# Optimization experiments

Measured on AMD Instinct MI355X. Metric: run time of the kernel, lower is better.

## Reference

```python
import jax, jax.numpy as jnp
import numpy as np

IMG = 128          # img_size
P = 8              # patch_size
H = 768            # model dim (hidden_size)
E = 1536           # GAU expansion dim (2*H), u/v width
K = 128            # key_size
L = (IMG // P) ** 2   # 256 patches
PD = P * P * 3        # 192 patch dim
T = 1000
NL = 24


def sinusoidal_embeddings(pos, dim, base):
    # pos: (L,) -> (L, dim) = [sin | cos]
    half = dim // 2
    freqs = jnp.exp(jnp.arange(half, dtype=jnp.float32) * (-np.log(base) / (half - 1)))
    ang = pos[:, None].astype(jnp.float32) * freqs[None, :]
    return jnp.concatenate([jnp.sin(ang), jnp.cos(ang)], axis=-1)


def make_rope_2d():
    w = IMG // P
    pos = jnp.arange(w * w)
    emb1 = sinusoidal_embeddings(pos // w, 64, 1000.0)
    emb2 = sinusoidal_embeddings(pos % w, 64, 1000.0)
    return jnp.concatenate([emb1, emb2], axis=-1)[None]  # (1, L, 128)


def apply_rope(x, pe):
    # faithful to source: sin_emb = pe[..., :d/2], cos_emb = pe[..., d/2:]
    d = pe.shape[-1]
    sin = pe[..., : d // 2]
    cos = pe[..., d // 2 :]
    x1 = x[..., : d // 2]
    x2 = x[..., d // 2 : d]
    return jnp.concatenate([x1 * cos - x2 * sin, x2 * cos + x1 * sin], axis=-1)


def rmsnorm(x, w):
    rms = jnp.sqrt(jnp.mean(x * x, axis=-1, keepdims=True))
    return x / (rms + 1e-6) * w


def setup_inputs() -> dict:
    key = jax.random.key(0)
    ks = jax.random.split(key, 9)
    B = 16
    s = 0.02
    return {
        "x": jax.random.normal(ks[0], (B, 3, IMG, IMG), dtype=jnp.float32),
        "t_idx": jax.random.randint(ks[1], (B, 1), 0, T),
        "patch_W": jax.random.normal(ks[2], (PD, H), dtype=jnp.float32) * s,
        "t_emb": jax.random.normal(ks[3], (T, H), dtype=jnp.float32) * s,
        "Wuv": jax.random.normal(ks[4], (NL, H, 2 * E + 2 * K), dtype=jnp.float32) * s,
        "Wout": jax.random.normal(ks[5], (NL, E, H), dtype=jnp.float32) * s,
        "gnorm": jnp.ones((NL, H), dtype=jnp.float32),
        "fnorm_w": jnp.ones((H,), dtype=jnp.float32),
        "unpatch_W": jax.random.normal(ks[6], (H, PD), dtype=jnp.float32) * s,
    }


def reference(x, t_idx, patch_W, t_emb, Wuv, Wout, gnorm, fnorm_w, unpatch_W):
    B = x.shape[0]
    g = IMG // P
    # patchify: (B,3,128,128) -> (B, 256, 192)
    xp = x.reshape(B, 3, g, P, g, P).transpose(0, 2, 4, 3, 5, 1).reshape(B, L, PD)
    h = xp @ patch_W + t_emb[t_idx[:, 0]][:, None, :]   # (B, L, H)
    pe = make_rope_2d()                                  # (1, L, 128)
    scale = K ** (-0.5)

    def block(h, params):
        wuv, wout, gn = params
        xn = rmsnorm(h, gn)
        uvqk = xn @ wuv                                  # (B, L, 2E+2K)
        u = jax.nn.silu(uvqk[..., :E])
        v = jax.nn.silu(uvqk[..., E : 2 * E])
        q = apply_rope(uvqk[..., 2 * E : 2 * E + K], pe)
        k = apply_rope(uvqk[..., 2 * E + K :], pe)
        attn = jax.nn.softmax(jnp.einsum('blk,bmk->blm', q, k) * scale, axis=-1)
        o = u * jnp.einsum('blm,bme->ble', attn, v)      # (B, L, E)
        return h + o @ wout, None

    h, _ = jax.lax.scan(block, h, (Wuv, Wout, gnorm))
    h = rmsnorm(h, fnorm_w) @ unpatch_W                  # (B, L, PD)
    # unpatchify: (B,256,192) -> (B,3,128,128)
    out = h.reshape(B, g, g, P, P, 3).transpose(0, 5, 1, 3, 2, 4).reshape(B, 3, IMG, IMG)
    return out
```

## Files before the change

kernel.cpp:

```cpp
#include <hip/hip_runtime.h>
#include <math.h>

#define IMG   128
#define Hdim  768
#define Edim  1536
#define Ltok  256
#define PDim  192
#define NLAY  24
#define Bsz   16
#define Mrows 4096
#define UVW   3328

typedef __bf16 bf16x8 __attribute__((ext_vector_type(8)));
typedef float  f32x4  __attribute__((ext_vector_type(4)));

__device__ __forceinline__ unsigned short f2b(float f) {
    unsigned int u = __float_as_uint(f);
    unsigned int r = (u + 0x7FFF + ((u >> 16) & 1)) >> 16;
    return (unsigned short)r;
}
__device__ __forceinline__ float b2f(unsigned short s) {
    return __uint_as_float((unsigned int)s << 16);
}
__device__ __forceinline__ unsigned int pk2(float lo, float hi) {
    return (unsigned int)f2b(lo) | ((unsigned int)f2b(hi) << 16);
}
__device__ __forceinline__ float silu(float x) {
    return x / (1.0f + expf(-x));
}
__device__ __forceinline__ void gload16(const void* g, void* l) {
    __builtin_amdgcn_global_load_lds(
        (const __attribute__((address_space(1))) void*)g,
        (__attribute__((address_space(3))) void*)l, 16, 0, 0);
}
__device__ __forceinline__ int xcd_wg() {
    int nwg = gridDim.x;
    int orig = blockIdx.x;
    int q8 = nwg >> 3, r8 = nwg & 7;
    int xcd = orig & 7, loc = orig >> 3;
    return (xcd < r8 ? xcd * (q8 + 1) : r8 * (q8 + 1) + (xcd - r8) * q8) + loc;
}

__global__ void pe_kernel(float* __restrict__ pe) {
    int l = blockIdx.x;
    int j = threadIdx.x;
    const float c = -logf(1000.0f) / 31.0f;
    int   sub = j & 31;
    float f   = expf(c * (float)sub);
    float pos = (j < 64) ? (float)(l >> 4) : (float)(l & 15);
    float ang = pos * f;
    pe[l * 128 + j] = ((j & 32) == 0) ? sinf(ang) : cosf(ang);
}

__global__ void patchify_kernel(const float* __restrict__ x, unsigned short* __restrict__ xp) {
    int bc = blockIdx.x;
    int iy = bc & 127;
    int t  = bc >> 7;
    int c  = t % 3;
    int b  = t / 3;
    int ix = threadIdx.x;
    float v = x[((size_t)(b * 3 + c) * IMG + iy) * IMG + ix];
    int gy = iy >> 3, py = iy & 7, gx = ix >> 3, px = ix & 7;
    xp[(size_t)(b * Ltok + gy * 16 + gx) * PDim + (py * 8 + px) * 3 + c] = f2b(v);
}

__global__ void trans_kernel(const float* __restrict__ src, int ldS, long long sS,
                             unsigned short* __restrict__ dst, int ldD, long long sD) {
    src += (long long)blockIdx.z * sS;
    dst += (long long)blockIdx.z * sD;
    __shared__ float t[32][33];
    int c0 = blockIdx.x * 32, r0 = blockIdx.y * 32;
    int tx = threadIdx.x, ty = threadIdx.y;
#pragma unroll
    for (int i = 0; i < 4; ++i)
        t[ty + 8 * i][tx] = src[(size_t)(r0 + ty + 8 * i) * ldS + c0 + tx];
    __syncthreads();
#pragma unroll
    for (int i = 0; i < 4; ++i)
        dst[(size_t)(c0 + ty + 8 * i) * ldD + r0 + tx] = f2b(t[tx][ty + 8 * i]);
}

template <int ACC>
__launch_bounds__(256)
__global__ void gemm_bf16(const unsigned short* __restrict__ A, int lda,
                          const unsigned short* __restrict__ Bt, int ldb,
                          float* __restrict__ C, int ldc,
                          int Kt, int Nt, int nbx) {
    __shared__ unsigned short lsA[2][4096];
    __shared__ unsigned short lsB[2][4096];
    int wg = xcd_wg();
    int bx = wg % nbx, by = wg / nbx;
    int tid  = threadIdx.x;
    int lane = tid & 63, w = tid >> 6, wr = w >> 1, wc = w & 1;
    int row0 = by * 128, col0 = bx * 128;
    int fr = lane & 15, fk = (lane >> 4) * 8;
    f32x4 acc[4][4] = {};

    int c0 = tid, c1 = tid + 256;
    int ar0 = row0 + (c0 >> 2), ar1 = row0 + (c1 >> 2);
    int bn0 = col0 + (c0 >> 2), bn1 = col0 + (c1 >> 2);
    if (bn0 > Nt - 1) bn0 = Nt - 1;
    if (bn1 > Nt - 1) bn1 = Nt - 1;
    int ka0 = (c0 & 3) * 8, ka1 = (c1 & 3) * 8;

#define STAGE_G(buf, k0)                                                       \
    gload16(A  + (size_t)ar0 * lda + (k0) + ka0, &lsA[buf][c0 * 8]);           \
    gload16(A  + (size_t)ar1 * lda + (k0) + ka1, &lsA[buf][c1 * 8]);           \
    gload16(Bt + (size_t)bn0 * ldb + (k0) + ka0, &lsB[buf][c0 * 8]);           \
    gload16(Bt + (size_t)bn1 * ldb + (k0) + ka1, &lsB[buf][c1 * 8]);

    STAGE_G(0, 0);
    __syncthreads();
    int nt = Kt >> 5, cur = 0;
    for (int t = 0; t < nt; ++t) {
        if (t + 1 < nt) { STAGE_G(cur ^ 1, (t + 1) * 32); }
        bf16x8 af[4], bfr[4];
#pragma unroll
        for (int m = 0; m < 4; ++m)
            af[m] = *(const bf16x8*)(&lsA[cur][(wr * 64 + m * 16 + fr) * 32 + fk]);
#pragma unroll
        for (int n = 0; n < 4; ++n)
            bfr[n] = *(const bf16x8*)(&lsB[cur][(wc * 64 + n * 16 + fr) * 32 + fk]);
#pragma unroll
        for (int m = 0; m < 4; ++m)
#pragma unroll
            for (int n = 0; n < 4; ++n)
                acc[m][n] = __builtin_amdgcn_mfma_f32_16x16x32_bf16(af[m], bfr[n], acc[m][n], 0, 0, 0);
        __syncthreads();
        cur ^= 1;
    }
#undef STAGE_G

    int crow = (lane >> 4) * 4;
#pragma unroll
    for (int m = 0; m < 4; ++m) {
#pragma unroll
        for (int n = 0; n < 4; ++n) {
            int gc = col0 + wc * 64 + n * 16 + fr;
            if (gc >= Nt) continue;
#pragma unroll
            for (int j = 0; j < 4; ++j) {
                size_t idx = (size_t)(row0 + wr * 64 + m * 16 + crow + j) * ldc + gc;
                if (ACC) C[idx] += acc[m][n][j];
                else     C[idx]  = acc[m][n][j];
            }
        }
    }
}

__launch_bounds__(256)
__global__ void gemm_wout(const unsigned short* __restrict__ A,
                          const unsigned short* __restrict__ Bt,
                          unsigned short* __restrict__ P) {
    __shared__ unsigned short lsA[2][4096];
    __shared__ unsigned short lsB[2][4096];
    int wg = xcd_wg();
    int sk = wg / 192, rem = wg % 192;
    int bx = rem % 6, by = rem / 6;
    int koff = sk * 384;
    unsigned short* C = P + (size_t)sk * Mrows * Hdim;
    int tid  = threadIdx.x;
    int lane = tid & 63, w = tid >> 6, wr = w >> 1, wc = w & 1;
    int row0 = by * 128, col0 = bx * 128;
    int fr = lane & 15, fk = (lane >> 4) * 8;
    f32x4 acc[4][4] = {};

    int c0 = tid, c1 = tid + 256;
    int ar0 = row0 + (c0 >> 2), ar1 = row0 + (c1 >> 2);
    int bn0 = col0 + (c0 >> 2), bn1 = col0 + (c1 >> 2);
    int ka0 = koff + (c0 & 3) * 8, ka1 = koff + (c1 & 3) * 8;

#define STAGE_W(buf, k0)                                                       \
    gload16(A  + (size_t)ar0 * Edim + (k0) + ka0, &lsA[buf][c0 * 8]);          \
    gload16(A  + (size_t)ar1 * Edim + (k0) + ka1, &lsA[buf][c1 * 8]);          \
    gload16(Bt + (size_t)bn0 * Edim + (k0) + ka0, &lsB[buf][c0 * 8]);          \
    gload16(Bt + (size_t)bn1 * Edim + (k0) + ka1, &lsB[buf][c1 * 8]);

    STAGE_W(0, 0);
    __syncthreads();
    int cur = 0;
    for (int t = 0; t < 12; ++t) {
        if (t + 1 < 12) { STAGE_W(cur ^ 1, (t + 1) * 32); }
        bf16x8 af[4], bfr[4];
#pragma unroll
        for (int m = 0; m < 4; ++m)
            af[m] = *(const bf16x8*)(&lsA[cur][(wr * 64 + m * 16 + fr) * 32 + fk]);
#pragma unroll
        for (int n = 0; n < 4; ++n)
            bfr[n] = *(const bf16x8*)(&lsB[cur][(wc * 64 + n * 16 + fr) * 32 + fk]);
#pragma unroll
        for (int m = 0; m < 4; ++m)
#pragma unroll
            for (int n = 0; n < 4; ++n)
                acc[m][n] = __builtin_amdgcn_mfma_f32_16x16x32_bf16(af[m], bfr[n], acc[m][n], 0, 0, 0);
        __syncthreads();
        cur ^= 1;
    }
#undef STAGE_W

    int crow = (lane >> 4) * 4;
#pragma unroll
    for (int m = 0; m < 4; ++m) {
#pragma unroll
        for (int n = 0; n < 4; ++n) {
            int gc = col0 + wc * 64 + n * 16 + fr;
#pragma unroll
            for (int j = 0; j < 4; ++j)
                C[(size_t)(row0 + wr * 64 + m * 16 + crow + j) * Hdim + gc] = f2b(acc[m][n][j]);
        }
    }
}

__global__ __launch_bounds__(512, 2)
void gemm_uvqk8(const unsigned short* __restrict__ A,
                const unsigned short* __restrict__ Bt,
                unsigned short* __restrict__ uT,
                unsigned short* __restrict__ vT,
                unsigned short* __restrict__ qh,
                unsigned short* __restrict__ kh,
                const float* __restrict__ pe) {
    __shared__ char smem[131072];
    int wg = xcd_wg();
    int bx = wg % 13, by = wg / 13;
    int tid = threadIdx.x, lane = tid & 63, wid = tid >> 6;
    int wm = wid >> 2, wn = wid & 3;
    int row0 = by * 256, col0 = bx * 256;
    int fr = lane & 15, hi = lane >> 4;
    f32x4 acc[8][4] = {};

    int d0 = tid * 16, d1 = d0 + 8192;
    int s0 = d0 ^ (((d0 >> 7) & 7) << 4);
    int s1 = d1 ^ (((d1 >> 7) & 7) << 4);
    int sr0 = s0 >> 7, sc0 = (s0 & 127) >> 1;
    int sr1 = s1 >> 7, sc1 = (s1 & 127) >> 1;

#define STG_A(bufo, h, kt) do {                                                            \
    gload16(A + (size_t)(row0 + (h) * 128 + sr0) * Hdim + (kt) * 64 + sc0,                 \
            smem + (bufo) + (h) * 16384 + d0);                                             \
    gload16(A + (size_t)(row0 + (h) * 128 + sr1) * Hdim + (kt) * 64 + sc1,                 \
            smem + (bufo) + (h) * 16384 + d1); } while (0)
#define STG_B(bufo, h, kt) do {                                                            \
    gload16(Bt + (size_t)(col0 + (h) * 128 + sr0) * Hdim + (kt) * 64 + sc0,                \
            smem + (bufo) + 32768 + (h) * 16384 + d0);                                     \
    gload16(Bt + (size_t)(col0 + (h) * 128 + sr1) * Hdim + (kt) * 64 + sc1,                \
            smem + (bufo) + 32768 + (h) * 16384 + d1); } while (0)

    int axor = (fr & 7) << 4;
    int abase = wm * 16384 + fr * 128;
    int bbase = 32768 + (wn >> 1) * 16384 + ((wn & 1) * 64 + fr) * 128;
    int koff0 = (hi * 16) ^ axor;
    int koff1 = (hi * 16 + 64) ^ axor;

    STG_A(0, 0, 0); STG_A(0, 1, 0); STG_B(0, 0, 0); STG_B(0, 1, 0);
    STG_A(65536, 0, 1); STG_A(65536, 1, 1);
    asm volatile("s_waitcnt vmcnt(4)" ::: "memory");
    __builtin_amdgcn_s_barrier();
    __builtin_amdgcn_sched_barrier(0);

    bf16x8 af[4][2], bf0[2][2], bf1[2][2];
    const int NKT = Hdim / 64;
    for (int kt = 0; kt < NKT; ++kt) {
        int curo = (kt & 1) << 16, nxto = curo ^ 65536;
        const char* bufc = smem + curo;

#pragma unroll
        for (int m = 0; m < 4; ++m) {
            af[m][0] = *(const bf16x8*)(bufc + abase + m * 2048 + koff0);
            af[m][1] = *(const bf16x8*)(bufc + abase + m * 2048 + koff1);
        }
#pragma unroll
        for (int n = 0; n < 2; ++n) {
            bf0[n][0] = *(const bf16x8*)(bufc + bbase + n * 2048 + koff0);
            bf0[n][1] = *(const bf16x8*)(bufc + bbase + n * 2048 + koff1);
        }
        if (kt + 1 < NKT) STG_B(nxto, 0, kt + 1);
        __builtin_amdgcn_s_setprio(1);
#pragma unroll
        for (int m = 0; m < 4; ++m)
#pragma unroll
            for (int n = 0; n < 2; ++n) {
                acc[m][n] = __builtin_amdgcn_mfma_f32_16x16x32_bf16(af[m][0], bf0[n][0], acc[m][n], 0, 0, 0);
                acc[m][n] = __builtin_amdgcn_mfma_f32_16x16x32_bf16(af[m][1], bf0[n][1], acc[m][n], 0, 0, 0);
            }
        __builtin_amdgcn_s_setprio(0);
        __builtin_amdgcn_s_barrier();
        __builtin_amdgcn_sched_barrier(0);

#pragma unroll
        for (int n = 0; n < 2; ++n) {
            bf1[n][0] = *(const bf16x8*)(bufc + bbase + (n + 2) * 2048 + koff0);
            bf1[n][1] = *(const bf16x8*)(bufc + bbase + (n + 2) * 2048 + koff1);
        }
        if (kt + 1 < NKT) STG_B(nxto, 1, kt + 1);
        __builtin_amdgcn_s_setprio(1);
#pragma unroll
        for (int m = 0; m < 4; ++m)
#pragma unroll
            for (int n = 0; n < 2; ++n) {
                acc[m][n + 2] = __builtin_amdgcn_mfma_f32_16x16x32_bf16(af[m][0], bf1[n][0], acc[m][n + 2], 0, 0, 0);
                acc[m][n + 2] = __builtin_amdgcn_mfma_f32_16x16x32_bf16(af[m][1], bf1[n][1], acc[m][n + 2], 0, 0, 0);
            }
        __builtin_amdgcn_s_setprio(0);
        __builtin_amdgcn_s_barrier();
        __builtin_amdgcn_sched_barrier(0);

#pragma unroll
        for (int m = 0; m < 4; ++m) {
            af[m][0] = *(const bf16x8*)(bufc + abase + (m + 4) * 2048 + koff0);
            af[m][1] = *(const bf16x8*)(bufc + abase + (m + 4) * 2048 + koff1);
        }
        __builtin_amdgcn_s_setprio(1);
#pragma unroll
        for (int m = 0; m < 4; ++m)
#pragma unroll
            for (int n = 0; n < 2; ++n) {
                acc[m + 4][n] = __builtin_amdgcn_mfma_f32_16x16x32_bf16(af[m][0], bf0[n][0], acc[m + 4][n], 0, 0, 0);
                acc[m + 4][n] = __builtin_amdgcn_mfma_f32_16x16x32_bf16(af[m][1], bf0[n][1], acc[m + 4][n], 0, 0, 0);
            }
        __builtin_amdgcn_s_setprio(0);
        __builtin_amdgcn_s_barrier();
        __builtin_amdgcn_sched_barrier(0);

        if (kt + 2 < NKT) { STG_A(curo, 0, kt + 2); STG_A(curo, 1, kt + 2); }
        __builtin_amdgcn_s_setprio(1);
#pragma unroll
        for (int m = 0; m < 4; ++m)
#pragma unroll
            for (int n = 0; n < 2; ++n) {
                acc[m + 4][n + 2] = __builtin_amdgcn_mfma_f32_16x16x32_bf16(af[m][0], bf1[n][0], acc[m + 4][n + 2], 0, 0, 0);
                acc[m + 4][n + 2] = __builtin_amdgcn_mfma_f32_16x16x32_bf16(af[m][1], bf1[n][1], acc[m + 4][n + 2], 0, 0, 0);
            }
        __builtin_amdgcn_s_setprio(0);
        asm volatile("s_waitcnt vmcnt(4)" ::: "memory");
        __builtin_amdgcn_s_barrier();
        __builtin_amdgcn_sched_barrier(0);
    }
#undef STG_A
#undef STG_B

    if (bx == 12) {
        float* S = (float*)smem;
        const float qscale = 0.08838834764831845f;
#pragma unroll
        for (int p = 0; p < 4; ++p) {
            __syncthreads();
            if (wm == (p >> 1)) {
#pragma unroll
                for (int m = 0; m < 4; ++m) {
                    int mf = (p & 1) * 4 + m;
                    int rl = m * 16 + hi * 4;
#pragma unroll
                    for (int n = 0; n < 4; ++n) {
                        int cl = wn * 64 + n * 16 + fr;
#pragma unroll
                        for (int j = 0; j < 4; ++j)
                            S[(rl + j) * 256 + cl] = acc[mf][n][j];
                    }
                }
            }
            __syncthreads();
            int r = tid >> 3;
            int dbase = (tid & 7) * 8;
            int row_g = row0 + p * 64 + r;
            int l = row_g & 255;
#pragma unroll
            for (int i = 0; i < 8; ++i) {
                int d = dbase + i;
                float sn = pe[l * 128 + d], cs = pe[l * 128 + 64 + d];
                float q1 = S[r * 256 + d],       q2 = S[r * 256 + d + 64];
                float k1 = S[r * 256 + d + 128], k2 = S[r * 256 + d + 192];
                qh[(size_t)row_g * 128 + d]      = f2b((q1 * cs - q2 * sn) * qscale);
                qh[(size_t)row_g * 128 + d + 64] = f2b((q2 * cs + q1 * sn) * qscale);
                kh[(size_t)row_g * 128 + d]      = f2b(k1 * cs - k2 * sn);
                kh[(size_t)row_g * 128 + d + 64] = f2b(k2 * cs + k1 * sn);
            }
        }
        return;
    }

    __syncthreads();
#pragma unroll
    for (int mf = 0; mf < 8; ++mf) {
        int m_l = wm * 128 + mf * 16 + hi * 4;
#pragma unroll
        for (int nf = 0; nf < 4; ++nf) {
            int e_l = wn * 64 + nf * 16 + fr;
            ushort4 pk;
            pk.x = f2b(silu(acc[mf][nf][0]));
            pk.y = f2b(silu(acc[mf][nf][1]));
            pk.z = f2b(silu(acc[mf][nf][2]));
            pk.w = f2b(silu(acc[mf][nf][3]));
            int byte = (e_l * 512 + m_l * 2) ^ ((e_l & 7) << 4);
            *(ushort4*)(smem + byte) = pk;
        }
    }
    __syncthreads();
    int er = tid >> 5;
    int ch = (tid & 31) * 16;
#pragma unroll
    for (int it = 0; it < 16; ++it) {
        int e_l = it * 16 + er;
        int byte = (e_l * 512 + ch) ^ ((e_l & 7) << 4);
        int4 v = *(const int4*)(smem + byte);
        unsigned short* dst;
        if (bx < 6) {
            dst = uT + (size_t)(col0 + e_l) * Mrows + row0;
        } else {
            int e = col0 + e_l - Edim;
            dst = vT + ((size_t)(row0 >> 8) * Edim + e) * Ltok;
        }
        *(int4*)((char*)dst + ch) = v;
    }
}

__launch_bounds__(256)
__global__ void fused_attn(const unsigned short* __restrict__ qh,
                           const unsigned short* __restrict__ kh,
                           const unsigned short* __restrict__ vT,
                           const unsigned short* __restrict__ uT,
                           unsigned short* __restrict__ ob) {
    int ec = blockIdx.x, qt = blockIdx.y, b = blockIdx.z;
    int tid  = threadIdx.x;
    int lane = tid & 63, w = tid >> 6;
    int fr = lane & 15, hi = lane >> 4;
    int qbase = b * 256 + qt * 64 + w * 16;

    bf16x8 qf[4];
#pragma unroll
    for (int ks = 0; ks < 4; ++ks)
        qf[ks] = *(const bf16x8*)(qh + (size_t)(qbase + fr) * 128 + ks * 32 + hi * 8);
    f32x4 sacc[16] = {};
#pragma unroll
    for (int mf = 0; mf < 16; ++mf) {
#pragma unroll
        for (int ks = 0; ks < 4; ++ks) {
            bf16x8 kf = *(const bf16x8*)(kh + (size_t)(b * 256 + mf * 16 + fr) * 128 + ks * 32 + hi * 8);
            sacc[mf] = __builtin_amdgcn_mfma_f32_16x16x32_bf16(kf, qf[ks], sacc[mf], 0, 0, 0);
        }
    }

    float mx = -3.4e38f;
#pragma unroll
    for (int mf = 0; mf < 16; ++mf)
#pragma unroll
        for (int j = 0; j < 4; ++j)
            mx = fmaxf(mx, sacc[mf][j]);
    mx = fmaxf(mx, __shfl_xor(mx, 16, 64));
    mx = fmaxf(mx, __shfl_xor(mx, 32, 64));
    float sum = 0.f;
#pragma unroll
    for (int mf = 0; mf < 16; ++mf)
#pragma unroll
        for (int j = 0; j < 4; ++j) {
            float e = expf(sacc[mf][j] - mx);
            sacc[mf][j] = e;
            sum += e;
        }
    sum += __shfl_xor(sum, 16, 64);
    sum += __shfl_xor(sum, 32, 64);
    float inv = 1.0f / sum;

    unsigned int dw[16][2];
#pragma unroll
    for (int mf = 0; mf < 16; ++mf) {
        dw[mf][0] = pk2(sacc[mf][0] * inv, sacc[mf][1] * inv);
        dw[mf][1] = pk2(sacc[mf][2] * inv, sacc[mf][3] * inv);
    }

    int sA = fr + 32 * (hi & 1);
    int sB = sA + 16;
    bool up = (hi >> 1) != 0;
    unsigned int pa[8][4];
#pragma unroll
    for (int ks = 0; ks < 8; ++ks) {
        unsigned int a00 = __shfl((int)dw[2 * ks][0],     sA, 64);
        unsigned int a01 = __shfl((int)dw[2 * ks + 1][0], sA, 64);
        unsigned int a10 = __shfl((int)dw[2 * ks][1],     sA, 64);
        unsigned int a11 = __shfl((int)dw[2 * ks + 1][1], sA, 64);
        unsigned int b00 = __shfl((int)dw[2 * ks][0],     sB, 64);
        unsigned int b01 = __shfl((int)dw[2 * ks + 1][0], sB, 64);
        unsigned int b10 = __shfl((int)dw[2 * ks][1],     sB, 64);
        unsigned int b11 = __shfl((int)dw[2 * ks + 1][1], sB, 64);
        pa[ks][0] = up ? a01 : a00;
        pa[ks][1] = up ? a11 : a10;
        pa[ks][2] = up ? b01 : b00;
        pa[ks][3] = up ? b11 : b10;
    }

    const unsigned short* vb = vT + (size_t)b * Edim * Ltok;
    int e0 = ec * 192;
#pragma unroll 2
    for (int ef = 0; ef < 12; ++ef) {
        int e = e0 + ef * 16 + fr;
        f32x4 oacc = {};
#pragma unroll
        for (int ks = 0; ks < 8; ++ks) {
            bf16x8 vf = *(const bf16x8*)(vb + (size_t)e * Ltok + ks * 32 + hi * 8);
            oacc = __builtin_amdgcn_mfma_f32_16x16x32_bf16(*(const bf16x8*)&pa[ks], vf, oacc, 0, 0, 0);
        }
        ushort4 uv = *(const ushort4*)(uT + (size_t)e * Mrows + qbase + hi * 4);
        ob[(size_t)(qbase + hi * 4 + 0) * Edim + e] = f2b(oacc[0] * b2f(uv.x));
        ob[(size_t)(qbase + hi * 4 + 1) * Edim + e] = f2b(oacc[1] * b2f(uv.y));
        ob[(size_t)(qbase + hi * 4 + 2) * Edim + e] = f2b(oacc[2] * b2f(uv.z));
        ob[(size_t)(qbase + hi * 4 + 3) * Edim + e] = f2b(oacc[3] * b2f(uv.w));
    }
}

__global__ void rmsnorm_bias(float* __restrict__ x, const float* __restrict__ t_emb,
                             const int* __restrict__ t_idx, const float* __restrict__ w,
                             unsigned short* __restrict__ y) {
    int r = blockIdx.x * 4 + (threadIdx.x >> 6);
    int lane = threadIdx.x & 63;
    const float* e = t_emb + (size_t)t_idx[r >> 8] * Hdim;
    float* xr = x + (size_t)r * Hdim;
    float4 a = *(const float4*)&xr[lane * 4];
    float4 b = *(const float4*)&xr[lane * 4 + 256];
    float4 c = *(const float4*)&xr[lane * 4 + 512];
    float4 ea = *(const float4*)&e[lane * 4];
    float4 eb = *(const float4*)&e[lane * 4 + 256];
    float4 ec = *(const float4*)&e[lane * 4 + 512];
    a.x += ea.x; a.y += ea.y; a.z += ea.z; a.w += ea.w;
    b.x += eb.x; b.y += eb.y; b.z += eb.z; b.w += eb.w;
    c.x += ec.x; c.y += ec.y; c.z += ec.z; c.w += ec.w;
    *(float4*)&xr[lane * 4]       = a;
    *(float4*)&xr[lane * 4 + 256] = b;
    *(float4*)&xr[lane * 4 + 512] = c;
    float ss = a.x * a.x + a.y * a.y + a.z * a.z + a.w * a.w
             + b.x * b.x + b.y * b.y + b.z * b.z + b.w * b.w
             + c.x * c.x + c.y * c.y + c.z * c.z + c.w * c.w;
#pragma unroll
    for (int o = 1; o < 64; o <<= 1) ss += __shfl_xor(ss, o, 64);
    float s = 1.0f / (sqrtf(ss / (float)Hdim) + 1e-6f);
    float4 wa = *(const float4*)&w[lane * 4];
    float4 wb = *(const float4*)&w[lane * 4 + 256];
    float4 wc = *(const float4*)&w[lane * 4 + 512];
    unsigned short* yr = y + (size_t)r * Hdim;
    ushort4 o0, o1, o2;
    o0.x = f2b(a.x * s * wa.x); o0.y = f2b(a.y * s * wa.y);
    o0.z = f2b(a.z * s * wa.z); o0.w = f2b(a.w * s * wa.w);
    o1.x = f2b(b.x * s * wb.x); o1.y = f2b(b.y * s * wb.y);
    o1.z = f2b(b.z * s * wb.z); o1.w = f2b(b.w * s * wb.w);
    o2.x = f2b(c.x * s * wc.x); o2.y = f2b(c.y * s * wc.y);
    o2.z = f2b(c.z * s * wc.z); o2.w = f2b(c.w * s * wc.w);
    *(ushort4*)&yr[lane * 4]       = o0;
    *(ushort4*)&yr[lane * 4 + 256] = o1;
    *(ushort4*)&yr[lane * 4 + 512] = o2;
}

__global__ void rmsnorm_acc(float* __restrict__ x, const unsigned short* __restrict__ p,
                            const float* __restrict__ w, unsigned short* __restrict__ y) {
    int r = blockIdx.x * 4 + (threadIdx.x >> 6);
    int lane = threadIdx.x & 63;
    float* xr = x + (size_t)r * Hdim;
    float4 a = *(const float4*)&xr[lane * 4];
    float4 b = *(const float4*)&xr[lane * 4 + 256];
    float4 c = *(const float4*)&xr[lane * 4 + 512];
#pragma unroll
    for (int s = 0; s < 4; ++s) {
        const unsigned short* ps = p + (size_t)(s * Mrows + r) * Hdim;
        ushort4 a0 = *(const ushort4*)&ps[lane * 4];
        ushort4 b0 = *(const ushort4*)&ps[lane * 4 + 256];
        ushort4 c0 = *(const ushort4*)&ps[lane * 4 + 512];
        a.x += b2f(a0.x); a.y += b2f(a0.y); a.z += b2f(a0.z); a.w += b2f(a0.w);
        b.x += b2f(b0.x); b.y += b2f(b0.y); b.z += b2f(b0.z); b.w += b2f(b0.w);
        c.x += b2f(c0.x); c.y += b2f(c0.y); c.z += b2f(c0.z); c.w += b2f(c0.w);
    }
    *(float4*)&xr[lane * 4]       = a;
    *(float4*)&xr[lane * 4 + 256] = b;
    *(float4*)&xr[lane * 4 + 512] = c;
    float ss = a.x * a.x + a.y * a.y + a.z * a.z + a.w * a.w
             + b.x * b.x + b.y * b.y + b.z * b.z + b.w * b.w
             + c.x * c.x + c.y * c.y + c.z * c.z + c.w * c.w;
#pragma unroll
    for (int o = 1; o < 64; o <<= 1) ss += __shfl_xor(ss, o, 64);
    float s = 1.0f / (sqrtf(ss / (float)Hdim) + 1e-6f);
    float4 wa = *(const float4*)&w[lane * 4];
    float4 wb = *(const float4*)&w[lane * 4 + 256];
    float4 wc = *(const float4*)&w[lane * 4 + 512];
    unsigned short* yr = y + (size_t)r * Hdim;
    ushort4 o0, o1, o2;
    o0.x = f2b(a.x * s * wa.x); o0.y = f2b(a.y * s * wa.y);
    o0.z = f2b(a.z * s * wa.z); o0.w = f2b(a.w * s * wa.w);
    o1.x = f2b(b.x * s * wb.x); o1.y = f2b(b.y * s * wb.y);
    o1.z = f2b(b.z * s * wb.z); o1.w = f2b(b.w * s * wb.w);
    o2.x = f2b(c.x * s * wc.x); o2.y = f2b(c.y * s * wc.y);
    o2.z = f2b(c.z * s * wc.z); o2.w = f2b(c.w * s * wc.w);
    *(ushort4*)&yr[lane * 4]       = o0;
    *(ushort4*)&yr[lane * 4 + 256] = o1;
    *(ushort4*)&yr[lane * 4 + 512] = o2;
}

__global__ void unpatch_kernel(const float* __restrict__ y, float* __restrict__ out) {
    int bc = blockIdx.x;
    int iy = bc & 127;
    int t  = bc >> 7;
    int c  = t % 3;
    int b  = t / 3;
    int ix = threadIdx.x;
    int gy = iy >> 3, py = iy & 7, gx = ix >> 3, px = ix & 7;
    out[((size_t)(b * 3 + c) * IMG + iy) * IMG + ix] =
        y[(size_t)(b * Ltok + gy * 16 + gx) * PDim + (py * 8 + px) * 3 + c];
}

extern "C" void kernel_launch(void* const* d_in, const int* in_sizes, int n_in,
                              void* d_out, int out_size, void* d_ws, size_t ws_size,
                              hipStream_t stream) {
    const float* x        = (const float*)d_in[0];
    const int*   t_idx    = (const int*)  d_in[1];
    const float* patch_W  = (const float*)d_in[2];
    const float* t_emb    = (const float*)d_in[3];
    const float* Wuv      = (const float*)d_in[4];
    const float* Wout     = (const float*)d_in[5];
    const float* gnorm    = (const float*)d_in[6];
    const float* fnorm    = (const float*)d_in[7];
    const float* unpatchW = (const float*)d_in[8];
    float* out = (float*)d_out;

    char* wsb = (char*)d_ws;
    size_t off = 0;
    auto alloc = [&](size_t bytes) { char* p = wsb + off; off += (bytes + 255) & ~(size_t)255; return p; };
    float* pe   = (float*)alloc(256 * 128 * 4);
    float* h    = (float*)alloc((size_t)Mrows * Hdim * 4);
    float* y    = (float*)alloc((size_t)Mrows * PDim * 4);
    unsigned short* pbuf = (unsigned short*)alloc((size_t)4 * Mrows * Hdim * 2);
    unsigned short* xp   = (unsigned short*)alloc((size_t)Mrows * PDim * 2);
    unsigned short* xn   = (unsigned short*)alloc((size_t)Mrows * Hdim * 2);
    unsigned short* uT   = (unsigned short*)alloc((size_t)Edim * Mrows * 2);
    unsigned short* vT   = (unsigned short*)alloc((size_t)Bsz * Edim * Ltok * 2);
    unsigned short* qh   = (unsigned short*)alloc((size_t)Mrows * 128 * 2);
    unsigned short* kh   = (unsigned short*)alloc((size_t)Mrows * 128 * 2);
    unsigned short* o_bf = (unsigned short*)alloc((size_t)Mrows * Edim * 2);
    unsigned short* WuvT  = (unsigned short*)alloc((size_t)NLAY * UVW * Hdim * 2);
    unsigned short* WoutT = (unsigned short*)alloc((size_t)NLAY * Hdim * Edim * 2);
    unsigned short* patchWT   = (unsigned short*)alloc((size_t)Hdim * PDim * 2);
    unsigned short* unpatchWT = (unsigned short*)alloc((size_t)PDim * Hdim * 2);
    if (off > ws_size) return;

    pe_kernel<<<256, 128, 0, stream>>>(pe);
    patchify_kernel<<<Bsz * 3 * IMG, IMG, 0, stream>>>(x, xp);

    trans_kernel<<<dim3(Hdim / 32, PDim / 32, 1), dim3(32, 8), 0, stream>>>(
        patch_W, Hdim, 0, patchWT, PDim, 0);
    trans_kernel<<<dim3(PDim / 32, Hdim / 32, 1), dim3(32, 8), 0, stream>>>(
        unpatchW, PDim, 0, unpatchWT, Hdim, 0);
    trans_kernel<<<dim3(UVW / 32, Hdim / 32, NLAY), dim3(32, 8), 0, stream>>>(
        Wuv, UVW, (long long)Hdim * UVW, WuvT, Hdim, (long long)UVW * Hdim);
    trans_kernel<<<dim3(Hdim / 32, Edim / 32, NLAY), dim3(32, 8), 0, stream>>>(
        Wout, Hdim, (long long)Edim * Hdim, WoutT, Edim, (long long)Hdim * Edim);

    gemm_bf16<0><<<(Hdim / 128) * (Mrows / 128), 256, 0, stream>>>(
        xp, PDim, patchWT, PDim, h, Hdim, PDim, Hdim, Hdim / 128);

    rmsnorm_bias<<<Mrows / 4, 256, 0, stream>>>(h, t_emb, t_idx, gnorm, xn);
    for (int l = 0; l < NLAY; ++l) {
        gemm_uvqk8<<<13 * (Mrows / 256), 512, 0, stream>>>(
            xn, WuvT + (size_t)l * UVW * Hdim, uT, vT, qh, kh, pe);
        fused_attn<<<dim3(8, 4, Bsz), 256, 0, stream>>>(qh, kh, vT, uT, o_bf);
        gemm_wout<<<768, 256, 0, stream>>>(
            o_bf, WoutT + (size_t)l * Hdim * Edim, pbuf);
        const float* nw = (l + 1 < NLAY) ? gnorm + (size_t)(l + 1) * Hdim : fnorm;
        rmsnorm_acc<<<Mrows / 4, 256, 0, stream>>>(h, pbuf, nw, xn);
    }

    gemm_bf16<0><<<2 * (Mrows / 128), 256, 0, stream>>>(
        xn, Hdim, unpatchWT, Hdim, y, PDim, Hdim, PDim, 2);
    unpatch_kernel<<<Bsz * 3 * IMG, IMG, 0, stream>>>(y, out);
}
```

Baseline: 2.685 ms.

## Store u row-major and stage epilogues through LDS for coalesced stores

The u activation now uses a row-major (token, E) layout instead of a transposed one. The uvqk GEMM writes it through a swizzled LDS tile as 16-byte row stores. The attention kernel stages its PV output in shared memory and multiplies by u with vectorized row-contiguous loads and stores, replacing scattered 2-byte stores. The Wout GEMM epilogue likewise goes through swizzled LDS for 16-byte coalesced writes. The aim is to cut uncoalesced global traffic, at the cost of extra LDS use (about 50KB in attention, which may lower occupancy) and extra barriers.

```diff
diff --git a/kernel.cpp b/kernel.cpp
--- a/kernel.cpp
+++ b/kernel.cpp
@@ -152,8 +152,9 @@
 __global__ void gemm_wout(const unsigned short* __restrict__ A,
                           const unsigned short* __restrict__ Bt,
                           unsigned short* __restrict__ P) {
-    __shared__ unsigned short lsA[2][4096];
-    __shared__ unsigned short lsB[2][4096];
+    __shared__ char smw[32768];
+    unsigned short (*lsA)[4096] = (unsigned short (*)[4096])smw;
+    unsigned short (*lsB)[4096] = (unsigned short (*)[4096])(smw + 16384);
     int wg = xcd_wg();
     int sk = wg / 192, rem = wg % 192;
     int bx = rem % 6, by = rem / 6;
@@ -199,22 +200,35 @@
 #undef STAGE_W
 
     int crow = (lane >> 4) * 4;
+    __syncthreads();
 #pragma unroll
     for (int m = 0; m < 4; ++m) {
 #pragma unroll
         for (int n = 0; n < 4; ++n) {
-            int gc = col0 + wc * 64 + n * 16 + fr;
-#pragma unroll
-            for (int j = 0; j < 4; ++j)
-                C[(size_t)(row0 + wr * 64 + m * 16 + crow + j) * Hdim + gc] = f2b(acc[m][n][j]);
-        }
+            int n_l = wc * 64 + n * 16 + fr;
+#pragma unroll
+            for (int j = 0; j < 4; ++j) {
+                int m_l = wr * 64 + m * 16 + crow + j;
+                int byte = (m_l * 256 + n_l * 2) ^ ((m_l & 7) << 4);
+                *(unsigned short*)(smw + byte) = f2b(acc[m][n][j]);
+            }
+        }
+    }
+    __syncthreads();
+    int grp = tid >> 4, l16 = tid & 15;
+#pragma unroll
+    for (int it = 0; it < 8; ++it) {
+        int r = it * 16 + grp;
+        int byte = (r * 256 + l16 * 16) ^ ((r & 7) << 4);
+        int4 v = *(const int4*)(smw + byte);
+        *(int4*)(C + (size_t)(row0 + r) * Hdim + col0 + l16 * 8) = v;
     }
 }
 
 __global__ __launch_bounds__(512, 2)
 void gemm_uvqk8(const unsigned short* __restrict__ A,
                 const unsigned short* __restrict__ Bt,
-                unsigned short* __restrict__ uT,
+                unsigned short* __restrict__ u_bf,
                 unsigned short* __restrict__ vT,
                 unsigned short* __restrict__ qh,
                 unsigned short* __restrict__ kh,
@@ -379,6 +393,33 @@
     }
 
     __syncthreads();
+    if (bx < 6) {
+#pragma unroll
+        for (int mf = 0; mf < 8; ++mf) {
+            int m0 = wm * 128 + mf * 16 + hi * 4;
+#pragma unroll
+            for (int nf = 0; nf < 4; ++nf) {
+                int e_l = wn * 64 + nf * 16 + fr;
+#pragma unroll
+                for (int j = 0; j < 4; ++j) {
+                    int m_l = m0 + j;
+                    int byte = (m_l * 512 + e_l * 2) ^ ((m_l & 7) << 4);
+                    *(unsigned short*)(smem + byte) = f2b(silu(acc[mf][nf][j]));
+                }
+            }
+        }
+        __syncthreads();
+        int grp = tid >> 5, l32 = tid & 31;
+#pragma unroll
+        for (int it = 0; it < 16; ++it) {
+            int r = it * 16 + grp;
+            int byte = (r * 512 + l32 * 16) ^ ((r & 7) << 4);
+            int4 v = *(const int4*)(smem + byte);
+            *(int4*)(u_bf + (size_t)(row0 + r) * Edim + bx * 256 + l32 * 8) = v;
+        }
+        return;
+    }
+
 #pragma unroll
     for (int mf = 0; mf < 8; ++mf) {
         int m_l = wm * 128 + mf * 16 + hi * 4;
@@ -395,20 +436,14 @@
         }
     }
     __syncthreads();
-    int er = tid >> 5;
-    int ch = (tid & 31) * 16;
+    int er = tid >> 5, ch = (tid & 31) * 16;
 #pragma unroll
     for (int it = 0; it < 16; ++it) {
         int e_l = it * 16 + er;
         int byte = (e_l * 512 + ch) ^ ((e_l & 7) << 4);
         int4 v = *(const int4*)(smem + byte);
-        unsigned short* dst;
-        if (bx < 6) {
-            dst = uT + (size_t)(col0 + e_l) * Mrows + row0;
-        } else {
-            int e = col0 + e_l - Edim;
-            dst = vT + ((size_t)(row0 >> 8) * Edim + e) * Ltok;
-        }
+        int e = col0 + e_l - Edim;
+        unsigned short* dst = vT + ((size_t)(row0 >> 8) * Edim + e) * Ltok;
         *(int4*)((char*)dst + ch) = v;
     }
 }
@@ -417,8 +452,9 @@
 __global__ void fused_attn(const unsigned short* __restrict__ qh,
                            const unsigned short* __restrict__ kh,
                            const unsigned short* __restrict__ vT,
-                           const unsigned short* __restrict__ uT,
+                           const unsigned short* __restrict__ u_bf,
                            unsigned short* __restrict__ ob) {
+    __shared__ float S[64 * 196];
     int ec = blockIdx.x, qt = blockIdx.y, b = blockIdx.z;
     int tid  = threadIdx.x;
     int lane = tid & 63, w = tid >> 6;
@@ -489,6 +525,7 @@
 
     const unsigned short* vb = vT + (size_t)b * Edim * Ltok;
     int e0 = ec * 192;
+    int rb = w * 16 + hi * 4;
 #pragma unroll 2
     for (int ef = 0; ef < 12; ++ef) {
         int e = e0 + ef * 16 + fr;
@@ -498,11 +535,32 @@
             bf16x8 vf = *(const bf16x8*)(vb + (size_t)e * Ltok + ks * 32 + hi * 8);
             oacc = __builtin_amdgcn_mfma_f32_16x16x32_bf16(*(const bf16x8*)&pa[ks], vf, oacc, 0, 0, 0);
         }
-        ushort4 uv = *(const ushort4*)(uT + (size_t)e * Mrows + qbase + hi * 4);
-        ob[(size_t)(qbase + hi * 4 + 0) * Edim + e] = f2b(oacc[0] * b2f(uv.x));
-        ob[(size_t)(qbase + hi * 4 + 1) * Edim + e] = f2b(oacc[1] * b2f(uv.y));
-        ob[(size_t)(qbase + hi * 4 + 2) * Edim + e] = f2b(oacc[2] * b2f(uv.z));
-        ob[(size_t)(qbase + hi * 4 + 3) * Edim + e] = f2b(oacc[3] * b2f(uv.w));
+        int el = ef * 16 + fr;
+        S[(rb + 0) * 196 + el] = oacc[0];
+        S[(rb + 1) * 196 + el] = oacc[1];
+        S[(rb + 2) * 196 + el] = oacc[2];
+        S[(rb + 3) * 196 + el] = oacc[3];
+    }
+    __syncthreads();
+
+    int r = tid >> 2, q = tid & 3;
+    size_t grow = (size_t)(b * 256 + qt * 64 + r);
+    const unsigned short* upv = u_bf + grow * Edim + e0 + q * 48;
+    unsigned short* opv = ob + grow * Edim + e0 + q * 48;
+    const float* Sr = S + r * 196 + q * 48;
+#pragma unroll
+    for (int i = 0; i < 6; ++i) {
+        float4 a = *(const float4*)(Sr + i * 8);
+        float4 c = *(const float4*)(Sr + i * 8 + 4);
+        ushort4 u0 = *(const ushort4*)(upv + i * 8);
+        ushort4 u1 = *(const ushort4*)(upv + i * 8 + 4);
+        ushort4 r0, r1;
+        r0.x = f2b(a.x * b2f(u0.x)); r0.y = f2b(a.y * b2f(u0.y));
+        r0.z = f2b(a.z * b2f(u0.z)); r0.w = f2b(a.w * b2f(u0.w));
+        r1.x = f2b(c.x * b2f(u1.x)); r1.y = f2b(c.y * b2f(u1.y));
+        r1.z = f2b(c.z * b2f(u1.z)); r1.w = f2b(c.w * b2f(u1.w));
+        *(ushort4*)(opv + i * 8) = r0;
+        *(ushort4*)(opv + i * 8 + 4) = r1;
     }
 }
 
@@ -625,7 +683,7 @@
     unsigned short* pbuf = (unsigned short*)alloc((size_t)4 * Mrows * Hdim * 2);
     unsigned short* xp   = (unsigned short*)alloc((size_t)Mrows * PDim * 2);
     unsigned short* xn   = (unsigned short*)alloc((size_t)Mrows * Hdim * 2);
-    unsigned short* uT   = (unsigned short*)alloc((size_t)Edim * Mrows * 2);
+    unsigned short* u_bf = (unsigned short*)alloc((size_t)Mrows * Edim * 2);
     unsigned short* vT   = (unsigned short*)alloc((size_t)Bsz * Edim * Ltok * 2);
     unsigned short* qh   = (unsigned short*)alloc((size_t)Mrows * 128 * 2);
     unsigned short* kh   = (unsigned short*)alloc((size_t)Mrows * 128 * 2);
@@ -654,8 +712,8 @@
     rmsnorm_bias<<<Mrows / 4, 256, 0, stream>>>(h, t_emb, t_idx, gnorm, xn);
     for (int l = 0; l < NLAY; ++l) {
         gemm_uvqk8<<<13 * (Mrows / 256), 512, 0, stream>>>(
-            xn, WuvT + (size_t)l * UVW * Hdim, uT, vT, qh, kh, pe);
-        fused_attn<<<dim3(8, 4, Bsz), 256, 0, stream>>>(qh, kh, vT, uT, o_bf);
+            xn, WuvT + (size_t)l * UVW * Hdim, u_bf, vT, qh, kh, pe);
+        fused_attn<<<dim3(8, 4, Bsz), 256, 0, stream>>>(qh, kh, vT, u_bf, o_bf);
         gemm_wout<<<768, 256, 0, stream>>>(
             o_bf, WoutT + (size_t)l * Hdim * Edim, pbuf);
         const float* nw = (l + 1 < NLAY) ? gnorm + (size_t)(l + 1) * Hdim : fnorm;
```

New measurement: 2.695 ms. No clear change (+0.4%).
